# Kernel tuning notes

Hardware: AMD Instinct MI355X
Metric: run time of the kernel (lower is better)

Reference implementation:

```python
import jax, jax.numpy as jnp
import numpy as np

K = 3          # hardcoded k in LocalHierarchicalFeature
BN_EPS = 1e-5  # torch BatchNorm2d default


def _fps(points, m):
    """Farthest point sampling: points [N, 5] -> m int32 indices (start at idx 0)."""
    n = points.shape[0]

    def body(i, carry):
        dist, mask, idxs = carry
        last = points[idxs[i - 1]]                      # [5]
        d = jnp.sum((points - last) ** 2, axis=-1)      # [N]
        dist = jnp.minimum(dist, d)
        dist = jnp.where(mask, -jnp.inf, dist)          # never reselect chosen points
        sel = jnp.argmax(dist).astype(jnp.int32)
        return dist, mask.at[sel].set(True), idxs.at[i].set(sel)

    dist0 = jnp.full((n,), jnp.inf, dtype=points.dtype)
    mask0 = jnp.zeros((n,), dtype=bool).at[0].set(True)
    idxs0 = jnp.zeros((m,), dtype=jnp.int32)
    _, _, idxs = jax.lax.fori_loop(1, m, body, (dist0, mask0, idxs0))
    return idxs


def _knn_idx(spatial_b, idxs, k):
    """Brute-force KNN of centroids against all points, excluding self. [M] -> [M, k]."""
    m = idxs.shape[0]
    cent = spatial_b[idxs]                                                   # [M, 5]
    d2 = jnp.sum((cent[:, None, :] - spatial_b[None, :, :]) ** 2, axis=-1)   # [M, N]
    d2 = d2.at[jnp.arange(m), idxs].set(-1.0)   # force self to be rank-0 in topk-smallest
    _, nn = jax.lax.top_k(-d2, k + 1)           # smallest k+1 distances
    return nn[:, 1:]                            # drop self -> [M, k]


def _forward(x, spatial, params):
    (W_sa, b_sa, bn_gamma, bn_beta, bn_mean, bn_var,
     W_in, b_in, W_q, b_q, W_k, b_k, W_v, b_v,
     W_w1, b_w1, W_w2, b_w2, W_out, b_out) = params
    B, N, _ = x.shape
    M = N // 2

    sp_sg = jax.lax.stop_gradient(spatial)  # indices are constants wrt differentiation
    idxs = jax.vmap(lambda p: _fps(p, M))(sp_sg)                    # [B, M]
    nn = jax.vmap(lambda p, i: _knn_idx(p, i, K))(sp_sg, idxs)      # [B, M, K]

    centroids = jax.vmap(lambda s, i: s[i])(spatial, idxs)          # [B, M, 5]
    nbr_feat = jax.vmap(lambda a, i: a[i])(x, nn)                   # [B, M, K, FD]
    nbr_sp = jax.vmap(lambda s, i: s[i])(spatial, nn)               # [B, M, K, 5]

    rel = nbr_sp - centroids[:, :, None, :]
    h = jnp.concatenate([nbr_feat, rel], axis=-1) @ W_sa + b_sa     # [B, M, K, AD]
    # BatchNorm2d(n_dim=M) in inference mode: channel dim is axis 1
    inv = bn_gamma / jnp.sqrt(bn_var + BN_EPS)
    scale = inv[None, :, None, None]
    shift = (bn_beta - bn_mean * inv)[None, :, None, None]
    f = jnp.max(jax.nn.relu(h * scale + shift), axis=2)             # max over K -> [B, M, AD]

    # vector attention (elementwise, per point)
    t = f @ W_in + b_in
    q = t @ W_q + b_q
    kk = t @ W_k + b_k
    v = t @ W_v + b_v
    w = jax.nn.softmax(jax.nn.relu((q - kk) @ W_w1 + b_w1) @ W_w2 + b_w2, axis=-1)
    out = (w * v) @ W_out + b_out + f                               # residual
    return out, centroids


def setup_inputs() -> dict:
    B, N, FD, AD, SD = 2, 8192, 64, 256, 5
    M = N // 2
    key = jax.random.key(0)
    ks = jax.random.split(key, 24)

    def lin(kw, kb, din, dout):
        s = 1.0 / np.sqrt(din)
        return (jax.random.uniform(kw, (din, dout), jnp.float32, -s, s),
                jax.random.uniform(kb, (dout,), jnp.float32, -s, s))

    W_sa, b_sa = lin(ks[0], ks[1], FD + SD, AD)
    W_in, b_in = lin(ks[2], ks[3], AD, AD)
    W_q, b_q = lin(ks[4], ks[5], AD, AD)
    W_k, b_k = lin(ks[6], ks[7], AD, AD)
    W_v, b_v = lin(ks[8], ks[9], AD, AD)
    W_w1, b_w1 = lin(ks[10], ks[11], AD, AD)
    W_w2, b_w2 = lin(ks[12], ks[13], AD, AD)
    W_out, b_out = lin(ks[14], ks[15], AD, AD)

    return {
        "x": jax.random.normal(ks[16], (B, N, FD), jnp.float32),
        "spatial": jax.random.normal(ks[17], (B, N, SD), jnp.float32),
        "W_sa": W_sa, "b_sa": b_sa,
        "bn_gamma": jax.random.uniform(ks[18], (M,), jnp.float32, 0.5, 1.5),
        "bn_beta": jax.random.normal(ks[19], (M,), jnp.float32) * 0.1,
        "bn_mean": jax.random.normal(ks[20], (M,), jnp.float32) * 0.1,
        "bn_var": jax.random.uniform(ks[21], (M,), jnp.float32, 0.5, 1.5),
        "W_in": W_in, "b_in": b_in, "W_q": W_q, "b_q": b_q,
        "W_k": W_k, "b_k": b_k, "W_v": W_v, "b_v": b_v,
        "W_w1": W_w1, "b_w1": b_w1, "W_w2": W_w2, "b_w2": b_w2,
        "W_out": W_out, "b_out": b_out,
    }


def reference(x, spatial, W_sa, b_sa, bn_gamma, bn_beta, bn_mean, bn_var,
              W_in, b_in, W_q, b_q, W_k, b_k, W_v, b_v,
              W_w1, b_w1, W_w2, b_w2, W_out, b_out):
    params = (W_sa, b_sa, bn_gamma, bn_beta, bn_mean, bn_var,
              W_in, b_in, W_q, b_q, W_k, b_k, W_v, b_v,
              W_w1, b_w1, W_w2, b_w2, W_out, b_out)
    return _forward(x, spatial, params)
```

## Files before the change

### kernel.cpp

```cpp
#include <hip/hip_runtime.h>
#include <math.h>

#define NPTS 8192
#define BATCH 2
#define MCENT 4096
#define FD 64
#define SD 5
#define AD 256

typedef float f32x2 __attribute__((ext_vector_type(2)));

#define FPS_T 1024
#define FPS_PAIRS 4

template<int CTRL>
__device__ __forceinline__ float dpp_max_f(float x) {
    const int o = __builtin_amdgcn_update_dpp(
        (int)0xff800000, __float_as_int(x), CTRL, 0xf, 0xf, false);
    return fmaxf(x, __int_as_float(o));
}
template<int CTRL>
__device__ __forceinline__ int dpp_min_i(int x) {
    const int o = __builtin_amdgcn_update_dpp(
        0x7fffffff, x, CTRL, 0xf, 0xf, false);
    return min(x, o);
}

__global__ __launch_bounds__(FPS_T) __attribute__((amdgpu_waves_per_eu(4, 4)))
void fps_kernel(const float* __restrict__ spatial, int* __restrict__ idxs)
{
#pragma clang fp contract(fast)
    const int b = blockIdx.x;
    const int tid = threadIdx.x;
    const float* sp = spatial + (size_t)b * NPTS * SD;
    int* out = idxs + (size_t)b * MCENT;

    __shared__ float cs0[NPTS];
    __shared__ float cs1[NPTS];
    __shared__ float cs2[NPTS];
    __shared__ float cs3[NPTS];
    __shared__ unsigned long long gk[2];

    for (int e = tid; e < NPTS; e += FPS_T) {
        cs0[e] = sp[(size_t)e * SD + 0];
        cs1[e] = sp[(size_t)e * SD + 1];
        cs2[e] = sp[(size_t)e * SD + 2];
        cs3[e] = sp[(size_t)e * SD + 3];
    }
    if (tid == 0) { gk[0] = 0ull; gk[1] = 0ull; }

    f32x2 P0[FPS_PAIRS], P1[FPS_PAIRS], P2[FPS_PAIRS], P3[FPS_PAIRS], P4[FPS_PAIRS];
    f32x2 d2[FPS_PAIRS];
#pragma unroll
    for (int q = 0; q < FPS_PAIRS; ++q) {
        const int p0 = tid + ((2 * q) << 10);
        const int p1 = p0 + 1024;
        P0[q].x = sp[(size_t)p0 * SD + 0]; P0[q].y = sp[(size_t)p1 * SD + 0];
        P1[q].x = sp[(size_t)p0 * SD + 1]; P1[q].y = sp[(size_t)p1 * SD + 1];
        P2[q].x = sp[(size_t)p0 * SD + 2]; P2[q].y = sp[(size_t)p1 * SD + 2];
        P3[q].x = sp[(size_t)p0 * SD + 3]; P3[q].y = sp[(size_t)p1 * SD + 3];
        P4[q].x = sp[(size_t)p0 * SD + 4]; P4[q].y = sp[(size_t)p1 * SD + 4];
        d2[q].x = INFINITY; d2[q].y = INFINITY;
    }
#pragma unroll
    for (int q = 0; q < FPS_PAIRS; ++q) {
        asm volatile("" : "+v"(P0[q]));
        asm volatile("" : "+v"(P1[q]));
        asm volatile("" : "+v"(P2[q]));
        asm volatile("" : "+v"(P3[q]));
        asm volatile("" : "+v"(P4[q]));
    }

    if (tid == 0) { d2[0].x = -INFINITY; out[0] = 0; }

    float l0 = sp[0], l1 = sp[1], l2 = sp[2], l3 = sp[3], l4 = sp[4];
    const int lane = tid & 63;
    __syncthreads();

    for (int i = 1; i < MCENT; ++i) {
        const int par = i & 1;
        const f32x2 L0 = {l0, l0}, L1 = {l1, l1}, L2 = {l2, l2},
                    L3 = {l3, l3}, L4 = {l4, l4};

        f32x2 s03[FPS_PAIRS];
#pragma unroll
        for (int q = 0; q < FPS_PAIRS; ++q) {
            f32x2 dx = P0[q] - L0; f32x2 s = dx * dx;
            f32x2 dy = P1[q] - L1; s = s + dy * dy;
            f32x2 dz = P2[q] - L2; s = s + dz * dz;
            f32x2 dw = P3[q] - L3; s = s + dw * dw;
            s03[q] = s;
        }
        float bv = -INFINITY;
#pragma unroll
        for (int q = 0; q < FPS_PAIRS; ++q) {
            f32x2 du = P4[q] - L4;
            f32x2 s = s03[q] + du * du;
            f32x2 nd;
            nd.x = fminf(d2[q].x, s.x);
            nd.y = fminf(d2[q].y, s.y);
            d2[q] = nd;
            bv = fmaxf(bv, fmaxf(nd.x, nd.y));
        }
        int bi = 0x7fffffff;
#pragma unroll
        for (int q = FPS_PAIRS - 1; q >= 0; --q) {
            const int p0 = tid + ((2 * q) << 10);
            if (d2[q].y == bv) bi = p0 + 1024;
            if (d2[q].x == bv) bi = p0;
        }

        float m = bv;
        m = dpp_max_f<0x111>(m);
        m = dpp_max_f<0x112>(m);
        m = dpp_max_f<0x114>(m);
        m = dpp_max_f<0x118>(m);
        m = dpp_max_f<0x142>(m);
        m = dpp_max_f<0x143>(m);
        const float wm = __int_as_float(
            __builtin_amdgcn_readlane(__float_as_int(m), 63));
        int cand = (bv == wm) ? bi : 0x7fffffff;
        cand = dpp_min_i<0x111>(cand);
        cand = dpp_min_i<0x112>(cand);
        cand = dpp_min_i<0x114>(cand);
        cand = dpp_min_i<0x118>(cand);
        cand = dpp_min_i<0x142>(cand);
        cand = dpp_min_i<0x143>(cand);
        const int wi = __builtin_amdgcn_readlane(cand, 63);

        if (lane == 0) {
            unsigned long long key =
                (((unsigned long long)(unsigned)__float_as_int(wm)) << 32)
                | (unsigned)(~wi);
            key ^= 0x8000000000000000ull;
            atomicMax(&gk[par], key);
        }
        if (tid == 0) gk[par ^ 1] = 0ull;
        __syncthreads();

        const unsigned long long k = gk[par];
        const int gidx = ~((int)(unsigned)k);
        const int su = __builtin_amdgcn_readfirstlane(gidx);
        l4 = sp[(size_t)su * SD + 4];
        l0 = cs0[su]; l1 = cs1[su]; l2 = cs2[su]; l3 = cs3[su];
        if (tid == 0) out[i] = gidx;
        const int dlt = gidx - tid;
#pragma unroll
        for (int q = 0; q < FPS_PAIRS; ++q) {
            if (dlt == ((2 * q) << 10))     d2[q].x = -INFINITY;
            if (dlt == ((2 * q + 1) << 10)) d2[q].y = -INFINITY;
        }
    }
}

#define KPARTS 8
__global__ __launch_bounds__(512) void knn_kernel(const float* __restrict__ spatial,
                                                  const int* __restrict__ idxs,
                                                  int* __restrict__ nn)
{
#pragma clang fp contract(off)
    const int blk = blockIdx.x;
    const int b = blk >> 6;
    const int grp = blk & 63;
    const int tid = threadIdx.x;
    const int lc = tid >> 3;
    const int part = tid & 7;
    const float* sp = spatial + (size_t)b * NPTS * SD;
    const int cid = (grp << 6) + lc;
    const int ctr = idxs[b * MCENT + cid];
    const float c0 = sp[(size_t)ctr * SD + 0], c1 = sp[(size_t)ctr * SD + 1],
                c2 = sp[(size_t)ctr * SD + 2], c3 = sp[(size_t)ctr * SD + 3],
                c4 = sp[(size_t)ctr * SD + 4];

    float bd[4] = {INFINITY, INFINITY, INFINITY, INFINITY};
    int   bi[4] = {0x7fffffff, 0x7fffffff, 0x7fffffff, 0x7fffffff};

    __shared__ float tile[2048 * SD];
    __shared__ float md[64][KPARTS][4];
    __shared__ int   mi[64][KPARTS][4];

    for (int t0 = 0; t0 < NPTS; t0 += 2048) {
        __syncthreads();
        for (int e = tid; e < 2048 * SD; e += 512) tile[e] = sp[(size_t)t0 * SD + e];
        __syncthreads();
        for (int p = part; p < 2048; p += KPARTS) {
            const int gp = t0 + p;
            float x0 = tile[p * SD + 0] - c0; float d = x0 * x0;
            float x1 = tile[p * SD + 1] - c1; d = d + x1 * x1;
            float x2 = tile[p * SD + 2] - c2; d = d + x2 * x2;
            float x3 = tile[p * SD + 3] - c3; d = d + x3 * x3;
            float x4 = tile[p * SD + 4] - c4; d = d + x4 * x4;
            if (gp == ctr) d = -1.0f;
            const bool lt0 = (d < bd[0]) || (d == bd[0] && gp < bi[0]);
            const bool lt1 = (d < bd[1]) || (d == bd[1] && gp < bi[1]);
            const bool lt2 = (d < bd[2]) || (d == bd[2] && gp < bi[2]);
            const bool lt3 = (d < bd[3]) || (d == bd[3] && gp < bi[3]);
            if (lt3) {
                bd[3] = lt2 ? bd[2] : d;  bi[3] = lt2 ? bi[2] : gp;
                if (lt2) {
                    bd[2] = lt1 ? bd[1] : d;  bi[2] = lt1 ? bi[1] : gp;
                    if (lt1) {
                        bd[1] = lt0 ? bd[0] : d;  bi[1] = lt0 ? bi[0] : gp;
                        if (lt0) { bd[0] = d; bi[0] = gp; }
                    }
                }
            }
        }
    }
#pragma unroll
    for (int s = 0; s < 4; ++s) { md[lc][part][s] = bd[s]; mi[lc][part][s] = bi[s]; }
    __syncthreads();
    if (part == 0) {
        int ptr[KPARTS] = {0, 0, 0, 0, 0, 0, 0, 0};
        int outi[4];
        for (int s = 0; s < 4; ++s) {
            float bestd = INFINITY; int besti = 0x7fffffff; int bl = 0;
            for (int l = 0; l < KPARTS; ++l) {
                const int pl = ptr[l];
                if (pl < 4) {
                    const float dv = md[lc][l][pl];
                    const int   iv = mi[lc][l][pl];
                    if (dv < bestd || (dv == bestd && iv < besti)) { bestd = dv; besti = iv; bl = l; }
                }
            }
            ptr[bl]++;
            outi[s] = besti;
        }
        int* o = nn + ((size_t)b * MCENT + cid) * 3;
        o[0] = outi[1]; o[1] = outi[2]; o[2] = outi[3];
    }
}

__global__ __launch_bounds__(256) void gather_kernel(const float* __restrict__ x,
                                                     const float* __restrict__ spatial,
                                                     const int* __restrict__ idxs,
                                                     const int* __restrict__ nn,
                                                     float* __restrict__ Asa,
                                                     float* __restrict__ cent_out)
{
    const int r = blockIdx.x;
    const int b = r >> 12;
    const int tid = threadIdx.x;
    const float* sp = spatial + (size_t)b * NPTS * SD;
    const float* xb = x + (size_t)b * NPTS * FD;
    const int ctr = idxs[r];
    __shared__ int nnk[3];
    if (tid < 3) nnk[tid] = nn[(size_t)r * 3 + tid];
    __syncthreads();
    if (tid < 192) {
        const int k = tid >> 6, c = tid & 63;
        Asa[((size_t)r * 3 + k) * 69 + c] = xb[(size_t)nnk[k] * FD + c];
    } else if (tid < 207) {
        const int e = tid - 192; const int k = e / 5, c = e % 5;
        Asa[((size_t)r * 3 + k) * 69 + 64 + c] =
            sp[(size_t)nnk[k] * SD + c] - sp[(size_t)ctr * SD + c];
    } else if (tid < 212) {
        const int c = tid - 207;
        cent_out[(size_t)r * SD + c] = sp[(size_t)ctr * SD + c];
    }
}

template<int EPI>
__global__ __launch_bounds__(256) void gemm_kernel(const float* __restrict__ A,
                                                   const float* __restrict__ Bw,
                                                   const float* __restrict__ bias,
                                                   const float* __restrict__ extra,
                                                   float* __restrict__ C,
                                                   int Mrows, int Kdim, int Ncols)
{
    __shared__ float As[16][64];
    __shared__ float Bs[16][64];
    const int tid = threadIdx.x;
    const int tx = tid & 15, ty = tid >> 4;
    const int m0 = blockIdx.y << 6, n0 = blockIdx.x << 6;
    float acc[4][4] = {};
    for (int k0 = 0; k0 < Kdim; k0 += 16) {
#pragma unroll
        for (int i = 0; i < 4; ++i) {
            const int e = tid + (i << 8);
            const int col = e & 63, row = e >> 6;
            const int gk = k0 + row;
            As[row][col] = (gk < Kdim) ? A[(size_t)(m0 + col) * Kdim + gk] : 0.f;
            Bs[row][col] = (gk < Kdim) ? Bw[(size_t)gk * Ncols + n0 + col] : 0.f;
        }
        __syncthreads();
#pragma unroll
        for (int kk = 0; kk < 16; ++kk) {
            const float4 ra = *(const float4*)(&As[kk][ty << 2]);
            const float4 rb = *(const float4*)(&Bs[kk][tx << 2]);
            const float av[4] = {ra.x, ra.y, ra.z, ra.w};
            const float bv[4] = {rb.x, rb.y, rb.z, rb.w};
#pragma unroll
            for (int ii = 0; ii < 4; ++ii)
#pragma unroll
                for (int jj = 0; jj < 4; ++jj)
                    acc[ii][jj] = fmaf(av[ii], bv[jj], acc[ii][jj]);
        }
        __syncthreads();
    }
#pragma unroll
    for (int ii = 0; ii < 4; ++ii) {
        const int gm = m0 + (ty << 2) + ii;
#pragma unroll
        for (int jj = 0; jj < 4; ++jj) {
            const int gn = n0 + (tx << 2) + jj;
            float v = acc[ii][jj] + bias[gn];
            if (EPI == 1) v = fmaxf(v, 0.f);
            if (EPI == 2) v += extra[(size_t)gm * Ncols + gn];
            C[(size_t)gm * Ncols + gn] = v;
        }
    }
}

__global__ __launch_bounds__(256) void bnmax_kernel(const float* __restrict__ h,
                                                    const float* __restrict__ g,
                                                    const float* __restrict__ be,
                                                    const float* __restrict__ mu,
                                                    const float* __restrict__ var,
                                                    float* __restrict__ f)
{
    const int r = blockIdx.x;
    const int m = r & (MCENT - 1);
    const int c = threadIdx.x;
    const float inv = g[m] / sqrtf(var[m] + 1e-5f);
    const float shift = be[m] - mu[m] * inv;
    const size_t base = (size_t)r * 3 * AD + c;
    const float v0 = fmaxf(h[base] * inv + shift, 0.f);
    const float v1 = fmaxf(h[base + AD] * inv + shift, 0.f);
    const float v2 = fmaxf(h[base + 2 * AD] * inv + shift, 0.f);
    f[(size_t)r * AD + c] = fmaxf(v0, fmaxf(v1, v2));
}

__global__ void wdiff_kernel(const float* __restrict__ Wq, const float* __restrict__ bq,
                             const float* __restrict__ Wk, const float* __restrict__ bk,
                             float* __restrict__ Wqk, float* __restrict__ bqk)
{
    const int i = blockIdx.x * blockDim.x + threadIdx.x;
    if (i < AD * AD) Wqk[i] = Wq[i] - Wk[i];
    if (i < AD) bqk[i] = bq[i] - bk[i];
}

__global__ __launch_bounds__(256) void softmax_kernel(float* __restrict__ s)
{
    const int r = blockIdx.x;
    const int c = threadIdx.x;
    const int lane = c & 63, w = c >> 6;
    float v = s[(size_t)r * AD + c];
    float mx = v;
#pragma unroll
    for (int off = 1; off < 64; off <<= 1) mx = fmaxf(mx, __shfl_xor(mx, off, 64));
    __shared__ float sm[4];
    __shared__ float ss[4];
    if (lane == 0) sm[w] = mx;
    __syncthreads();
    mx = fmaxf(fmaxf(sm[0], sm[1]), fmaxf(sm[2], sm[3]));
    const float e = expf(v - mx);
    float sum = e;
#pragma unroll
    for (int off = 1; off < 64; off <<= 1) sum += __shfl_xor(sum, off, 64);
    if (lane == 0) ss[w] = sum;
    __syncthreads();
    sum = ss[0] + ss[1] + ss[2] + ss[3];
    s[(size_t)r * AD + c] = e / sum;
}

__global__ void mul_kernel(const float* __restrict__ w, float* __restrict__ v, int n)
{
    for (int i = blockIdx.x * blockDim.x + threadIdx.x; i < n; i += gridDim.x * blockDim.x)
        v[i] = w[i] * v[i];
}

extern "C" void kernel_launch(void* const* d_in, const int* in_sizes, int n_in,
                              void* d_out, int out_size, void* d_ws, size_t ws_size,
                              hipStream_t stream)
{
    const float* x       = (const float*)d_in[0];
    const float* spatial = (const float*)d_in[1];
    const float* W_sa  = (const float*)d_in[2];
    const float* b_sa  = (const float*)d_in[3];
    const float* gamma = (const float*)d_in[4];
    const float* beta  = (const float*)d_in[5];
    const float* mean  = (const float*)d_in[6];
    const float* var   = (const float*)d_in[7];
    const float* W_in  = (const float*)d_in[8];
    const float* b_in  = (const float*)d_in[9];
    const float* W_q   = (const float*)d_in[10];
    const float* b_q   = (const float*)d_in[11];
    const float* W_k   = (const float*)d_in[12];
    const float* b_k   = (const float*)d_in[13];
    const float* W_v   = (const float*)d_in[14];
    const float* b_v   = (const float*)d_in[15];
    const float* W_w1  = (const float*)d_in[16];
    const float* b_w1  = (const float*)d_in[17];
    const float* W_w2  = (const float*)d_in[18];
    const float* b_w2  = (const float*)d_in[19];
    const float* W_out = (const float*)d_in[20];
    const float* b_out = (const float*)d_in[21];

    float* ws = (float*)d_ws;
    size_t o = 0;
    int* idxs = (int*)(ws + o); o += BATCH * MCENT;
    int* nn   = (int*)(ws + o); o += BATCH * MCENT * 3;
    float* Wqk = ws + o; o += AD * AD;
    float* bqk = ws + o; o += AD;
    float* Asa = ws + o; o += (size_t)BATCH * MCENT * 3 * 69;
    float* h   = ws + o; o += (size_t)BATCH * MCENT * 3 * AD;
    float* f   = ws + o; o += (size_t)BATCH * MCENT * AD;
    float* u   = ws + o; o += (size_t)BATCH * MCENT * AD;
    float* t   = h;
    float* qd  = h + (size_t)BATCH * MCENT * AD;
    float* v   = h + (size_t)2 * BATCH * MCENT * AD;
    float* sgm = qd;

    float* outp = (float*)d_out;
    float* cent = outp + (size_t)BATCH * MCENT * AD;

    const int ROWS = BATCH * MCENT;
    const int HROWS = ROWS * 3;

    fps_kernel<<<BATCH, FPS_T, 0, stream>>>(spatial, idxs);
    knn_kernel<<<BATCH * 64, 512, 0, stream>>>(spatial, idxs, nn);
    gather_kernel<<<ROWS, 256, 0, stream>>>(x, spatial, idxs, nn, Asa, cent);
    wdiff_kernel<<<(AD * AD + 255) / 256, 256, 0, stream>>>(W_q, b_q, W_k, b_k, Wqk, bqk);

    gemm_kernel<0><<<dim3(AD / 64, HROWS / 64), 256, 0, stream>>>(Asa, W_sa, b_sa, nullptr, h, HROWS, 69, AD);
    bnmax_kernel<<<ROWS, 256, 0, stream>>>(h, gamma, beta, mean, var, f);
    gemm_kernel<0><<<dim3(AD / 64, ROWS / 64), 256, 0, stream>>>(f, W_in, b_in, nullptr, t, ROWS, AD, AD);
    gemm_kernel<0><<<dim3(AD / 64, ROWS / 64), 256, 0, stream>>>(t, Wqk, bqk, nullptr, qd, ROWS, AD, AD);
    gemm_kernel<0><<<dim3(AD / 64, ROWS / 64), 256, 0, stream>>>(t, W_v, b_v, nullptr, v, ROWS, AD, AD);
    gemm_kernel<1><<<dim3(AD / 64, ROWS / 64), 256, 0, stream>>>(qd, W_w1, b_w1, nullptr, u, ROWS, AD, AD);
    gemm_kernel<0><<<dim3(AD / 64, ROWS / 64), 256, 0, stream>>>(u, W_w2, b_w2, nullptr, sgm, ROWS, AD, AD);
    softmax_kernel<<<ROWS, 256, 0, stream>>>(sgm);
    mul_kernel<<<2048, 256, 0, stream>>>(sgm, v, ROWS * AD);
    gemm_kernel<2><<<dim3(AD / 64, ROWS / 64), 256, 0, stream>>>(v, W_out, b_out, f, outp, ROWS, AD, AD);
}
```

Before: 5.316 ms.

## Use bf16 MFMA in GEMM kernel and fuse softmax with value multiply

Rewrites the tiled GEMM to convert fp32 tiles to bf16 in shared memory and compute with 16x16x32 bf16 MFMA instructions, four accumulators per wave. Separately fuses the softmax and the elementwise multiply into one kernel to avoid an extra pass over memory. This reduces GEMM compute cost at the price of bf16 input precision, which may affect accuracy.

```diff
diff --git a/kernel.cpp b/kernel.cpp
--- a/kernel.cpp
+++ b/kernel.cpp
@@ -9,6 +9,8 @@
 #define AD 256
 
 typedef float f32x2 __attribute__((ext_vector_type(2)));
+typedef float f32x4 __attribute__((ext_vector_type(4)));
+typedef short short8 __attribute__((ext_vector_type(8)));
 
 #define FPS_T 1024
 #define FPS_PAIRS 4
@@ -260,6 +262,12 @@
     }
 }
 
+__device__ __forceinline__ unsigned short f2bf(float f) {
+    const unsigned u = __float_as_uint(f);
+    const unsigned r = ((u >> 16) & 1u) + 0x7fffu;
+    return (unsigned short)((u + r) >> 16);
+}
+
 template<int EPI>
 __global__ __launch_bounds__(256) void gemm_kernel(const float* __restrict__ A,
                                                    const float* __restrict__ Bw,
@@ -268,47 +276,56 @@
                                                    float* __restrict__ C,
                                                    int Mrows, int Kdim, int Ncols)
 {
-    __shared__ float As[16][64];
-    __shared__ float Bs[16][64];
+    __shared__ unsigned short As[64][40];
+    __shared__ unsigned short Bs[64][40];
     const int tid = threadIdx.x;
-    const int tx = tid & 15, ty = tid >> 4;
     const int m0 = blockIdx.y << 6, n0 = blockIdx.x << 6;
-    float acc[4][4] = {};
-    for (int k0 = 0; k0 < Kdim; k0 += 16) {
-#pragma unroll
-        for (int i = 0; i < 4; ++i) {
-            const int e = tid + (i << 8);
-            const int col = e & 63, row = e >> 6;
-            const int gk = k0 + row;
-            As[row][col] = (gk < Kdim) ? A[(size_t)(m0 + col) * Kdim + gk] : 0.f;
-            Bs[row][col] = (gk < Kdim) ? Bw[(size_t)gk * Ncols + n0 + col] : 0.f;
-        }
+    const int w = tid >> 6, l = tid & 63;
+    const int wm0 = (w >> 1) << 5, wn0 = (w & 1) << 5;
+    const int fr = l & 15;
+    const int fk = l >> 4;
+
+    f32x4 acc[2][2] = {};
+
+    const int arow = tid >> 2, akc = (tid & 3) << 3;
+    const int bn = tid & 63, bkg = (tid >> 6) << 3;
+
+    for (int k0 = 0; k0 < Kdim; k0 += 32) {
         __syncthreads();
 #pragma unroll
-        for (int kk = 0; kk < 16; ++kk) {
-            const float4 ra = *(const float4*)(&As[kk][ty << 2]);
-            const float4 rb = *(const float4*)(&Bs[kk][tx << 2]);
-            const float av[4] = {ra.x, ra.y, ra.z, ra.w};
-            const float bv[4] = {rb.x, rb.y, rb.z, rb.w};
-#pragma unroll
-            for (int ii = 0; ii < 4; ++ii)
-#pragma unroll
-                for (int jj = 0; jj < 4; ++jj)
-                    acc[ii][jj] = fmaf(av[ii], bv[jj], acc[ii][jj]);
+        for (int j = 0; j < 8; ++j) {
+            const int gk = k0 + akc + j;
+            const float vv = (gk < Kdim) ? A[(size_t)(m0 + arow) * Kdim + gk] : 0.f;
+            As[arow][akc + j] = f2bf(vv);
+        }
+#pragma unroll
+        for (int j = 0; j < 8; ++j) {
+            const int gk = k0 + bkg + j;
+            const float vv = (gk < Kdim) ? Bw[(size_t)gk * Ncols + n0 + bn] : 0.f;
+            Bs[bn][bkg + j] = f2bf(vv);
         }
         __syncthreads();
-    }
-#pragma unroll
-    for (int ii = 0; ii < 4; ++ii) {
-        const int gm = m0 + (ty << 2) + ii;
-#pragma unroll
-        for (int jj = 0; jj < 4; ++jj) {
-            const int gn = n0 + (tx << 2) + jj;
-            float v = acc[ii][jj] + bias[gn];
-            if (EPI == 1) v = fmaxf(v, 0.f);
-            if (EPI == 2) v += extra[(size_t)gm * Ncols + gn];
-            C[(size_t)gm * Ncols + gn] = v;
-        }
+        const short8 a0 = *(const short8*)&As[wm0 + fr][fk << 3];
+        const short8 a1 = *(const short8*)&As[wm0 + 16 + fr][fk << 3];
+        const short8 b0 = *(const short8*)&Bs[wn0 + fr][fk << 3];
+        const short8 b1 = *(const short8*)&Bs[wn0 + 16 + fr][fk << 3];
+        acc[0][0] = __builtin_amdgcn_mfma_f32_16x16x32_bf16(a0, b0, acc[0][0], 0, 0, 0);
+        acc[0][1] = __builtin_amdgcn_mfma_f32_16x16x32_bf16(a0, b1, acc[0][1], 0, 0, 0);
+        acc[1][0] = __builtin_amdgcn_mfma_f32_16x16x32_bf16(a1, b0, acc[1][0], 0, 0, 0);
+        acc[1][1] = __builtin_amdgcn_mfma_f32_16x16x32_bf16(a1, b1, acc[1][1], 0, 0, 0);
+    }
+#pragma unroll
+    for (int r = 0; r < 2; ++r)
+#pragma unroll
+    for (int c = 0; c < 2; ++c)
+#pragma unroll
+    for (int j = 0; j < 4; ++j) {
+        const int gm = m0 + wm0 + (r << 4) + (fk << 2) + j;
+        const int gn = n0 + wn0 + (c << 4) + fr;
+        float vv = acc[r][c][j] + bias[gn];
+        if (EPI == 1) vv = fmaxf(vv, 0.f);
+        if (EPI == 2) vv += extra[(size_t)gm * Ncols + gn];
+        C[(size_t)gm * Ncols + gn] = vv;
     }
 }
 
@@ -340,13 +357,15 @@
     if (i < AD) bqk[i] = bq[i] - bk[i];
 }
 
-__global__ __launch_bounds__(256) void softmax_kernel(float* __restrict__ s)
+__global__ __launch_bounds__(256) void softmax_mul_kernel(const float* __restrict__ s,
+                                                          float* __restrict__ v)
 {
     const int r = blockIdx.x;
     const int c = threadIdx.x;
     const int lane = c & 63, w = c >> 6;
-    float v = s[(size_t)r * AD + c];
-    float mx = v;
+    const size_t idx = (size_t)r * AD + c;
+    const float x = s[idx];
+    float mx = x;
 #pragma unroll
     for (int off = 1; off < 64; off <<= 1) mx = fmaxf(mx, __shfl_xor(mx, off, 64));
     __shared__ float sm[4];
@@ -354,20 +373,14 @@
     if (lane == 0) sm[w] = mx;
     __syncthreads();
     mx = fmaxf(fmaxf(sm[0], sm[1]), fmaxf(sm[2], sm[3]));
-    const float e = expf(v - mx);
+    const float e = expf(x - mx);
     float sum = e;
 #pragma unroll
     for (int off = 1; off < 64; off <<= 1) sum += __shfl_xor(sum, off, 64);
     if (lane == 0) ss[w] = sum;
     __syncthreads();
     sum = ss[0] + ss[1] + ss[2] + ss[3];
-    s[(size_t)r * AD + c] = e / sum;
-}
-
-__global__ void mul_kernel(const float* __restrict__ w, float* __restrict__ v, int n)
-{
-    for (int i = blockIdx.x * blockDim.x + threadIdx.x; i < n; i += gridDim.x * blockDim.x)
-        v[i] = w[i] * v[i];
+    v[idx] = (e / sum) * v[idx];
 }
 
 extern "C" void kernel_launch(void* const* d_in, const int* in_sizes, int n_in,
@@ -430,7 +443,6 @@
     gemm_kernel<0><<<dim3(AD / 64, ROWS / 64), 256, 0, stream>>>(t, W_v, b_v, nullptr, v, ROWS, AD, AD);
     gemm_kernel<1><<<dim3(AD / 64, ROWS / 64), 256, 0, stream>>>(qd, W_w1, b_w1, nullptr, u, ROWS, AD, AD);
     gemm_kernel<0><<<dim3(AD / 64, ROWS / 64), 256, 0, stream>>>(u, W_w2, b_w2, nullptr, sgm, ROWS, AD, AD);
-    softmax_kernel<<<ROWS, 256, 0, stream>>>(sgm);
-    mul_kernel<<<2048, 256, 0, stream>>>(sgm, v, ROWS * AD);
+    softmax_mul_kernel<<<ROWS, 256, 0, stream>>>(sgm, v);
     gemm_kernel<2><<<dim3(AD / 64, ROWS / 64), 256, 0, stream>>>(v, W_out, b_out, f, outp, ROWS, AD, AD);
 }
```

Measured after the change: 5.315 ms. No clear change (-0.0%).
